# Performance work log

Measured on AMD Instinct MI355X. Metric: run time of the kernel, lower is better.

## Reference

```python
import jax, jax.numpy as jnp
import numpy as np

N_BLOCKS = 4
IN_C = 1024
N_EMBED = 8192
BATCH = 8192
BETA = 1.0
BN_EPS = 1e-5


def _l2norm(t, axis=-1):
    return t / jnp.clip(jnp.linalg.norm(t, axis=axis, keepdims=True), 1e-12, None)


def _mlp_blocks(x, W, b, g, be):
    # n_blocks x (Linear -> BatchNorm1d (batch stats) -> ReLU)
    for i in range(W.shape[0]):
        h = x @ W[i].T + b[i]
        m = h.mean(axis=0)
        v = h.var(axis=0)  # biased var, as torch BN training
        h = (h - m) / jnp.sqrt(v + BN_EPS) * g[i] + be[i]
        x = jax.nn.relu(h)
    return x


def _vq_layer(x, W1, b1, W2, b2):
    return jnp.tanh(x @ W1.T + b1) @ W2.T + b2


def setup_inputs() -> dict:
    key = jax.random.key(0)
    ks = jax.random.split(key, 16)
    w = lambda k, shape: 0.01 * jax.random.normal(k, shape, dtype=jnp.float32)
    d = {
        "x": jax.random.normal(ks[0], (BATCH, IN_C), dtype=jnp.float32),
        "enc_W": w(ks[1], (N_BLOCKS, IN_C, IN_C)),
        "enc_b": jnp.zeros((N_BLOCKS, IN_C), jnp.float32),
        "enc_g": jnp.ones((N_BLOCKS, IN_C), jnp.float32),
        "enc_be": jnp.zeros((N_BLOCKS, IN_C), jnp.float32),
        "enc_vW1": w(ks[2], (IN_C, IN_C)),
        "enc_vb1": jnp.zeros((IN_C,), jnp.float32),
        "enc_vW2": w(ks[3], (IN_C, IN_C)),
        "enc_vb2": jnp.zeros((IN_C,), jnp.float32),
        "dec_W": w(ks[4], (N_BLOCKS, IN_C, IN_C)),
        "dec_b": jnp.zeros((N_BLOCKS, IN_C), jnp.float32),
        "dec_g": jnp.ones((N_BLOCKS, IN_C), jnp.float32),
        "dec_be": jnp.zeros((N_BLOCKS, IN_C), jnp.float32),
        "dec_vW1": w(ks[5], (IN_C, IN_C)),
        "dec_vb1": jnp.zeros((IN_C,), jnp.float32),
        "dec_vW2": w(ks[6], (IN_C, IN_C)),
        "dec_vb2": jnp.zeros((IN_C,), jnp.float32),
        "codebook": _l2norm(jax.random.normal(ks[7], (N_EMBED, IN_C), dtype=jnp.float32)),
    }
    return d


def reference(x, enc_W, enc_b, enc_g, enc_be, enc_vW1, enc_vb1, enc_vW2, enc_vb2,
              dec_W, dec_b, dec_g, dec_be, dec_vW1, dec_vb1, dec_vW2, dec_vb2, codebook):
    # ---- encoder ----
    h = _mlp_blocks(x, enc_W, enc_b, enc_g, enc_be)
    z = _vq_layer(h, enc_vW1, enc_vb1, enc_vW2, enc_vb2)  # [B, D]

    # ---- NormEMA vector quantizer (eval math) ----
    z = _l2norm(z)
    e = _l2norm(codebook)  # [K, D]
    # d(i,k) = |z_i|^2 + |e_k|^2 - 2 z_i . e_k
    d = (jnp.sum(z * z, axis=1, keepdims=True)
         + jnp.sum(e * e, axis=1)[None, :]
         - 2.0 * z @ e.T)  # [B, K]
    idx = jnp.argmin(d, axis=1)
    z_q = e[idx]  # [B, D]
    emb_loss = BETA * jnp.mean((jax.lax.stop_gradient(z_q) - z) ** 2)
    z_q = z + jax.lax.stop_gradient(z_q - z)  # straight-through

    # ---- decoder ----
    h = _mlp_blocks(z_q, dec_W, dec_b, dec_g, dec_be)
    xrec = _vq_layer(h, dec_vW1, dec_vb1, dec_vW2, dec_vb2)
    return xrec, emb_loss
```

## Files before the change

### kernel.cpp

```cpp
#include <hip/hip_runtime.h>

typedef unsigned int u32;
typedef unsigned short u16;
typedef unsigned long long u64;

typedef __attribute__((ext_vector_type(8))) short short8;
typedef __attribute__((ext_vector_type(4))) float f32x4;
typedef __attribute__((ext_vector_type(8))) unsigned short u16x8;
typedef __attribute__((ext_vector_type(4))) unsigned short u16x4;

#define C_DIM 1024
#define B_ROWS 8192
#define N_EMB 8192
#define BN_EPS_C 1e-5f
#define KK 1024

__device__ __forceinline__ u16 f2bf_rne(float x) {
  u32 b = __float_as_uint(x);
  u32 r = b + 0x7fffu + ((b >> 16) & 1u);
  return (u16)(r >> 16);
}
__device__ __forceinline__ float bf2f(u16 h) {
  return __uint_as_float(((u32)h) << 16);
}

__device__ __forceinline__ void gl2lds(const u16* g, u16* l) {
  __builtin_amdgcn_global_load_lds(
      (const __attribute__((address_space(1))) void*)g,
      (__attribute__((address_space(3))) void*)l, 16, 0, 0);
}

__device__ __forceinline__ float block_reduce_sum_256(float v) {
#pragma unroll
  for (int off = 32; off > 0; off >>= 1) v += __shfl_xor(v, off, 64);
  __shared__ float sh[4];
  __syncthreads();
  const int lane = threadIdx.x & 63, w = threadIdx.x >> 6;
  if (lane == 0) sh[w] = v;
  __syncthreads();
  return (sh[0] + sh[1]) + (sh[2] + sh[3]);
}

__device__ __forceinline__ u64 shfl_xor_u64(u64 v, int m) {
  int lo = __shfl_xor((int)(u32)v, m, 64);
  int hi = __shfl_xor((int)(u32)(v >> 32), m, 64);
  return ((u64)(u32)hi << 32) | (u32)lo;
}

__global__ __launch_bounds__(256) void cvt4(
    const float* __restrict__ s0, u16* __restrict__ h0, u16* __restrict__ l0,
    int nb0, const float* __restrict__ s1, u16* __restrict__ h1,
    u16* __restrict__ l1, int nb1, const float* __restrict__ s2,
    u16* __restrict__ h2, u16* __restrict__ l2, int nb2,
    const float* __restrict__ s3, u16* __restrict__ h3, u16* __restrict__ l3) {
  int b = blockIdx.x;
  const float* s;
  u16 *h, *l;
  if (b < nb0) {
    s = s0; h = h0; l = l0;
  } else if (b < nb0 + nb1) {
    b -= nb0; s = s1; h = h1; l = l1;
  } else if (b < nb0 + nb1 + nb2) {
    b -= nb0 + nb1; s = s2; h = h2; l = l2;
  } else {
    b -= nb0 + nb1 + nb2; s = s3; h = h3; l = l3;
  }
  const int i = b * 256 + threadIdx.x;
  const float4 v = ((const float4*)s)[i];
  u16x4 hh, ll;
  hh.x = f2bf_rne(v.x); ll.x = f2bf_rne(v.x - bf2f(hh.x));
  hh.y = f2bf_rne(v.y); ll.y = f2bf_rne(v.y - bf2f(hh.y));
  hh.z = f2bf_rne(v.z); ll.z = f2bf_rne(v.z - bf2f(hh.z));
  hh.w = f2bf_rne(v.w); ll.w = f2bf_rne(v.w - bf2f(hh.w));
  ((u16x4*)h)[i] = hh;
  ((u16x4*)l)[i] = ll;
}

template <int WF32>
__global__ __launch_bounds__(256) void l2norm_ext(const float* __restrict__ in,
                                                  float* __restrict__ outF,
                                                  u16* __restrict__ outH,
                                                  u16* __restrict__ outL,
                                                  float* __restrict__ ssq,
                                                  u64* __restrict__ binit) {
  const int row = blockIdx.x;
  const float4 v = ((const float4*)(in + (size_t)row * C_DIM))[threadIdx.x];
  float ss = v.x * v.x + v.y * v.y + v.z * v.z + v.w * v.w;
  ss = block_reduce_sum_256(ss);
  float nrm = sqrtf(ss);
  nrm = fmaxf(nrm, 1e-12f);
  float4 o;
  o.x = v.x / nrm; o.y = v.y / nrm; o.z = v.z / nrm; o.w = v.w / nrm;
  if (WF32) ((float4*)(outF + (size_t)row * C_DIM))[threadIdx.x] = o;
  u16x4 h, l;
  h.x = f2bf_rne(o.x); l.x = f2bf_rne(o.x - bf2f(h.x));
  h.y = f2bf_rne(o.y); l.y = f2bf_rne(o.y - bf2f(h.y));
  h.z = f2bf_rne(o.z); l.z = f2bf_rne(o.z - bf2f(h.z));
  h.w = f2bf_rne(o.w); l.w = f2bf_rne(o.w - bf2f(h.w));
  ((u16x4*)(outH + (size_t)row * C_DIM))[threadIdx.x] = h;
  ((u16x4*)(outL + (size_t)row * C_DIM))[threadIdx.x] = l;
  float s2 = o.x * o.x + o.y * o.y + o.z * o.z + o.w * o.w;
  s2 = block_reduce_sum_256(s2);
  if (threadIdx.x == 0) {
    ssq[row] = s2;
    if (binit) binit[row] = ~0ull;
  }
}

template <int MODE, int TERMS, int CS, int TB>
__global__ __launch_bounds__(256, (TB ? 4 : 2)) void gemm_bf3(
    const u16* __restrict__ Ahg, const u16* __restrict__ Alg,
    const u16* __restrict__ Bhg, const u16* __restrict__ Blg,
    const float* __restrict__ bias, float* __restrict__ outF,
    u16* __restrict__ outH, u16* __restrict__ outL, float* __restrict__ cs1,
    float* __restrict__ cs2, const float* __restrict__ zz,
    u64* __restrict__ best, int N) {
  __shared__ __align__(16) u16 lds[16384];
  __shared__ float csum[CS ? 4 * 64 * 2 : 1];
  const int tid = threadIdx.x;
  const int lane = tid & 63, w = tid >> 6;
  const int wr = w >> 1, wc = w & 1;
  const int m0 = blockIdx.y * 128, n0 = blockIdx.x * 128;

  const int r0l = w * 32 + (lane >> 2);
  const int r1l = r0l + 16;
  const int c0 = (((lane & 3) ^ ((r0l >> 1) & 3)) << 3);
  const int c1 = (((lane & 3) ^ ((r1l >> 1) & 3)) << 3);
  const u16* pAh0 = Ahg + (size_t)(m0 + r0l) * KK + c0;
  const u16* pAh1 = Ahg + (size_t)(m0 + r1l) * KK + c1;
  const u16* pAl0 = Alg + (size_t)(m0 + r0l) * KK + c0;
  const u16* pAl1 = Alg + (size_t)(m0 + r1l) * KK + c1;
  const u16* pBh0 = Bhg + (size_t)(n0 + r0l) * KK + c0;
  const u16* pBh1 = Bhg + (size_t)(n0 + r1l) * KK + c1;
  const u16* pBl0 = Blg + (size_t)(n0 + r0l) * KK + c0;
  const u16* pBl1 = Blg + (size_t)(n0 + r1l) * KK + c1;
  u16* const db = lds + w * 1024;

  int oa[4], ob[4];
  const int q = lane >> 4;
#pragma unroll
  for (int t = 0; t < 4; ++t) {
    const int ra = wr * 64 + t * 16 + (lane & 15);
    oa[t] = ra * 32 + ((q ^ ((ra >> 1) & 3)) << 3);
    const int rb = wc * 64 + t * 16 + (lane & 15);
    ob[t] = rb * 32 + ((q ^ ((rb >> 1) & 3)) << 3);
  }

  f32x4 acc[4][4];
#pragma unroll
  for (int i = 0; i < 4; ++i)
#pragma unroll
    for (int j = 0; j < 4; ++j) acc[i][j] = (f32x4){0.f, 0.f, 0.f, 0.f};

  for (int k0 = 0; k0 < KK; k0 += 32) {
    __syncthreads();
    gl2lds(pAh0 + k0, db);
    gl2lds(pAh1 + k0, db + 512);
    gl2lds(pAl0 + k0, db + 4096);
    gl2lds(pAl1 + k0, db + 4608);
    gl2lds(pBh0 + k0, db + 8192);
    gl2lds(pBh1 + k0, db + 8704);
    gl2lds(pBl0 + k0, db + 12288);
    gl2lds(pBl1 + k0, db + 12800);
    asm volatile("s_waitcnt vmcnt(0)" ::: "memory");
    __syncthreads();

    if (TB) {
      short8 fa[4], fb[4], fx[4];
#pragma unroll
      for (int t = 0; t < 4; ++t) {
        fa[t] = *(const short8*)(lds + oa[t]);
        fb[t] = *(const short8*)(lds + 8192 + ob[t]);
      }
#pragma unroll
      for (int i = 0; i < 4; ++i)
#pragma unroll
        for (int j = 0; j < 4; ++j)
          acc[i][j] = __builtin_amdgcn_mfma_f32_16x16x32_bf16(
              fa[i], fb[j], acc[i][j], 0, 0, 0);
#pragma unroll
      for (int t = 0; t < 4; ++t)
        fx[t] = *(const short8*)(lds + 12288 + ob[t]);
#pragma unroll
      for (int i = 0; i < 4; ++i)
#pragma unroll
        for (int j = 0; j < 4; ++j)
          acc[i][j] = __builtin_amdgcn_mfma_f32_16x16x32_bf16(
              fa[i], fx[j], acc[i][j], 0, 0, 0);
#pragma unroll
      for (int t = 0; t < 4; ++t)
        fa[t] = *(const short8*)(lds + 4096 + oa[t]);
#pragma unroll
      for (int i = 0; i < 4; ++i)
#pragma unroll
        for (int j = 0; j < 4; ++j)
          acc[i][j] = __builtin_amdgcn_mfma_f32_16x16x32_bf16(
              fa[i], fb[j], acc[i][j], 0, 0, 0);
      if (TERMS == 4) {
#pragma unroll
        for (int i = 0; i < 4; ++i)
#pragma unroll
          for (int j = 0; j < 4; ++j)
            acc[i][j] = __builtin_amdgcn_mfma_f32_16x16x32_bf16(
                fa[i], fx[j], acc[i][j], 0, 0, 0);
      }
    } else {
      short8 ah[4], al[4], bh[4], bl[4];
#pragma unroll
      for (int t = 0; t < 4; ++t) {
        ah[t] = *(const short8*)(lds + oa[t]);
        al[t] = *(const short8*)(lds + 4096 + oa[t]);
        bh[t] = *(const short8*)(lds + 8192 + ob[t]);
        bl[t] = *(const short8*)(lds + 12288 + ob[t]);
      }
#pragma unroll
      for (int i = 0; i < 4; ++i)
#pragma unroll
        for (int j = 0; j < 4; ++j) {
          acc[i][j] = __builtin_amdgcn_mfma_f32_16x16x32_bf16(
              ah[i], bh[j], acc[i][j], 0, 0, 0);
          acc[i][j] = __builtin_amdgcn_mfma_f32_16x16x32_bf16(
              ah[i], bl[j], acc[i][j], 0, 0, 0);
          acc[i][j] = __builtin_amdgcn_mfma_f32_16x16x32_bf16(
              al[i], bh[j], acc[i][j], 0, 0, 0);
          if (TERMS == 4)
            acc[i][j] = __builtin_amdgcn_mfma_f32_16x16x32_bf16(
                al[i], bl[j], acc[i][j], 0, 0, 0);
        }
    }
  }

  const int rbase = m0 + wr * 64 + (lane >> 4) * 4;
  const int cbase = n0 + wc * 64 + (lane & 15);

  if (MODE == 2) {
    float sev[4];
#pragma unroll
    for (int j = 0; j < 4; ++j) sev[j] = bias[cbase + j * 16];
#pragma unroll
    for (int i = 0; i < 4; ++i)
#pragma unroll
      for (int v = 0; v < 4; ++v) {
        const int row = rbase + i * 16 + v;
        const float zr = zz[row];
        u64 bkey = ~0ull;
#pragma unroll
        for (int j = 0; j < 4; ++j) {
          const float d = (zr + sev[j]) - 2.0f * acc[i][j][v];
          const u32 fb2 = __float_as_uint(d);
          const u32 k32 = (fb2 & 0x80000000u) ? ~fb2 : (fb2 | 0x80000000u);
          const u64 key = ((u64)k32 << 32) | (u32)(cbase + j * 16);
          bkey = (key < bkey) ? key : bkey;
        }
#pragma unroll
        for (int mm = 1; mm < 16; mm <<= 1) {
          const u64 o = shfl_xor_u64(bkey, mm);
          bkey = (o < bkey) ? o : bkey;
        }
        if ((lane & 15) == 0) atomicMin(best + row, bkey);
      }
  } else {
    float bb[4];
#pragma unroll
    for (int j = 0; j < 4; ++j) bb[j] = bias[cbase + j * 16];
    float s[4] = {0.f, 0.f, 0.f, 0.f}, ss[4] = {0.f, 0.f, 0.f, 0.f};
#pragma unroll
    for (int i = 0; i < 4; ++i)
#pragma unroll
      for (int j = 0; j < 4; ++j)
#pragma unroll
        for (int v = 0; v < 4; ++v) {
          const int row = rbase + i * 16 + v;
          const int col = cbase + j * 16;
          float val = acc[i][j][v] + bb[j];
          if (MODE == 1) {
            val = tanhf(val);
            const u16 h = f2bf_rne(val);
            outH[(size_t)row * N + col] = h;
            outL[(size_t)row * N + col] = f2bf_rne(val - bf2f(h));
          } else {
            outF[(size_t)row * N + col] = val;
            if (CS) {
              s[j] += val;
              ss[j] += val * val;
            }
          }
        }
    if (CS) {
#pragma unroll
      for (int j = 0; j < 4; ++j) {
        s[j] += __shfl_xor(s[j], 16, 64);
        s[j] += __shfl_xor(s[j], 32, 64);
        ss[j] += __shfl_xor(ss[j], 16, 64);
        ss[j] += __shfl_xor(ss[j], 32, 64);
      }
      if (lane < 16) {
#pragma unroll
        for (int j = 0; j < 4; ++j) {
          csum[(w * 64 + j * 16 + lane) * 2 + 0] = s[j];
          csum[(w * 64 + j * 16 + lane) * 2 + 1] = ss[j];
        }
      }
      __syncthreads();
      if (tid < 128) {
        const int col = tid;
        const int wcc = col >> 6, idx = col & 63;
        const float S = csum[(wcc * 64 + idx) * 2 + 0] +
                        csum[((2 + wcc) * 64 + idx) * 2 + 0];
        const float SS = csum[(wcc * 64 + idx) * 2 + 1] +
                         csum[((2 + wcc) * 64 + idx) * 2 + 1];
        cs1[(size_t)blockIdx.y * C_DIM + n0 + col] = S;
        cs2[(size_t)blockIdx.y * C_DIM + n0 + col] = SS;
      }
    }
  }
}

__global__ __launch_bounds__(256) void bn_stats2(const float* __restrict__ cs1,
                                                 const float* __restrict__ cs2,
                                                 const float* __restrict__ g,
                                                 float* __restrict__ mean,
                                                 float* __restrict__ scale) {
  const int c = blockIdx.x * 256 + threadIdx.x;
  float s = 0.f, ss = 0.f;
  for (int i = 0; i < 64; ++i) {
    s += cs1[i * C_DIM + c];
    ss += cs2[i * C_DIM + c];
  }
  const float m = s * (1.0f / 8192.0f);
  const float v = ss * (1.0f / 8192.0f) - m * m;
  mean[c] = m;
  scale[c] = g[c] / sqrtf(v + BN_EPS_C);
}

__global__ __launch_bounds__(256) void bn_relu_cvt(
    const float* __restrict__ t, const float* __restrict__ mean,
    const float* __restrict__ scale, const float* __restrict__ be,
    u16* __restrict__ outH, u16* __restrict__ outL) {
  const int i = blockIdx.x * 256 + threadIdx.x;
  const int c4 = i & 255;
  const float4 v = ((const float4*)t)[i];
  const float4 m = ((const float4*)mean)[c4];
  const float4 sc = ((const float4*)scale)[c4];
  const float4 b = ((const float4*)be)[c4];
  float4 r;
  r.x = fmaxf((v.x - m.x) * sc.x + b.x, 0.f);
  r.y = fmaxf((v.y - m.y) * sc.y + b.y, 0.f);
  r.z = fmaxf((v.z - m.z) * sc.z + b.z, 0.f);
  r.w = fmaxf((v.w - m.w) * sc.w + b.w, 0.f);
  u16x4 h, l;
  h.x = f2bf_rne(r.x); l.x = f2bf_rne(r.x - bf2f(h.x));
  h.y = f2bf_rne(r.y); l.y = f2bf_rne(r.y - bf2f(h.y));
  h.z = f2bf_rne(r.z); l.z = f2bf_rne(r.z - bf2f(h.z));
  h.w = f2bf_rne(r.w); l.w = f2bf_rne(r.w - bf2f(h.w));
  ((u16x4*)outH)[i] = h;
  ((u16x4*)outL)[i] = l;
}

__global__ __launch_bounds__(256) void gather_zq_cvt(
    const float* __restrict__ z, const u16* __restrict__ eh,
    const u16* __restrict__ el, const u64* __restrict__ best,
    u16* __restrict__ zqh, u16* __restrict__ zql, float* __restrict__ rowp) {
  const int row = blockIdx.x;
  const u32 idx = (u32)(best[row] & 0xffffffffu);
  const float4 zv = ((const float4*)(z + (size_t)row * C_DIM))[threadIdx.x];
  const u16x4 evh = ((const u16x4*)(eh + (size_t)idx * C_DIM))[threadIdx.x];
  const u16x4 evl = ((const u16x4*)(el + (size_t)idx * C_DIM))[threadIdx.x];
  float4 ev;
  ev.x = bf2f(evh.x) + bf2f(evl.x);
  ev.y = bf2f(evh.y) + bf2f(evl.y);
  ev.z = bf2f(evh.z) + bf2f(evl.z);
  ev.w = bf2f(evh.w) + bf2f(evl.w);
  float4 d, o;
  d.x = ev.x - zv.x; d.y = ev.y - zv.y; d.z = ev.z - zv.z; d.w = ev.w - zv.w;
  o.x = zv.x + d.x; o.y = zv.y + d.y; o.z = zv.z + d.z; o.w = zv.w + d.w;
  u16x4 h, l;
  h.x = f2bf_rne(o.x); l.x = f2bf_rne(o.x - bf2f(h.x));
  h.y = f2bf_rne(o.y); l.y = f2bf_rne(o.y - bf2f(h.y));
  h.z = f2bf_rne(o.z); l.z = f2bf_rne(o.z - bf2f(h.z));
  h.w = f2bf_rne(o.w); l.w = f2bf_rne(o.w - bf2f(h.w));
  ((u16x4*)(zqh + (size_t)row * C_DIM))[threadIdx.x] = h;
  ((u16x4*)(zql + (size_t)row * C_DIM))[threadIdx.x] = l;
  float ss = d.x * d.x + d.y * d.y + d.z * d.z + d.w * d.w;
  ss = block_reduce_sum_256(ss);
  if (threadIdx.x == 0) rowp[row] = ss;
}

__global__ __launch_bounds__(256) void embloss_fin(const float* __restrict__ rowp,
                                                   float* __restrict__ out) {
  float s = 0.f;
  for (int i = threadIdx.x; i < B_ROWS; i += 256) s += rowp[i];
  s = block_reduce_sum_256(s);
  if (threadIdx.x == 0) out[0] = s * (1.0f / (8192.0f * 1024.0f));
}

extern "C" void kernel_launch(void* const* d_in, const int* in_sizes, int n_in,
                              void* d_out, int out_size, void* d_ws,
                              size_t ws_size, hipStream_t stream) {
  const float* x = (const float*)d_in[0];
  const float* enc_W = (const float*)d_in[1];
  const float* enc_b = (const float*)d_in[2];
  const float* enc_g = (const float*)d_in[3];
  const float* enc_be = (const float*)d_in[4];
  const float* enc_vW1 = (const float*)d_in[5];
  const float* enc_vb1 = (const float*)d_in[6];
  const float* enc_vW2 = (const float*)d_in[7];
  const float* enc_vb2 = (const float*)d_in[8];
  const float* dec_W = (const float*)d_in[9];
  const float* dec_b = (const float*)d_in[10];
  const float* dec_g = (const float*)d_in[11];
  const float* dec_be = (const float*)d_in[12];
  const float* dec_vW1 = (const float*)d_in[13];
  const float* dec_vb1 = (const float*)d_in[14];
  const float* dec_vW2 = (const float*)d_in[15];
  const float* dec_vb2 = (const float*)d_in[16];
  const float* cb = (const float*)d_in[17];

  const size_t NE = (size_t)B_ROWS * C_DIM;
  const size_t WN = (size_t)C_DIM * C_DIM;
  float* ws = (float*)d_ws;
  float* R1 = ws;
  float* R2 = R1 + NE;
  float* R3 = R2 + NE;
  float* R4 = R3 + NE;
  float* se = R4 + NE;
  float* zz = se + N_EMB;
  u64* best = (u64*)(zz + B_ROWS);
  float* cs1 = (float*)(best + B_ROWS);
  float* cs2 = cs1 + 64 * C_DIM;
  float* mean = cs2 + 64 * C_DIM;
  float* scal = mean + C_DIM;
  float* rowp = scal + C_DIM;

  u16* wa = (u16*)R4;
  u16* ehi = (u16*)R4;
  u16* elo = ehi + NE;
  u16* xh = (u16*)R2;
  u16* xl = xh + NE;
  u16* aH = (u16*)R2;
  u16* aL = aH + NE;
  u16* bH = (u16*)R3;
  u16* bL = bH + NE;
  u16* zhi = (u16*)R2;
  u16* zlo = zhi + NE;
  float* zf = R1;

  float* xrec = (float*)d_out;
  float* loss = xrec + NE;

  const dim3 blk(256);
  const dim3 gemmGrid(C_DIM / 128, B_ROWS / 128);
  const dim3 distGrid(N_EMB / 128, B_ROWS / 128);
  const dim3 s2Grid(C_DIM / 256);
  const dim3 brGrid(B_ROWS * C_DIM / 1024);

  cvt4<<<dim3(4096 + 1024 + 1024 + 8192), blk, 0, stream>>>(
      enc_W, wa, wa + 4 * WN, 4096, enc_vW1, wa + 8 * WN, wa + 9 * WN, 1024,
      enc_vW2, wa + 10 * WN, wa + 11 * WN, 1024, x, xh, xl);

  gemm_bf3<0, 4, 1, 0><<<gemmGrid, blk, 0, stream>>>(
      xh, xl, wa, wa + 4 * WN, enc_b, R1, nullptr, nullptr, cs1, cs2, nullptr,
      nullptr, C_DIM);
  bn_stats2<<<s2Grid, blk, 0, stream>>>(cs1, cs2, enc_g, mean, scal);
  bn_relu_cvt<<<brGrid, blk, 0, stream>>>(R1, mean, scal, enc_be, bH, bL);

  gemm_bf3<0, 4, 1, 0><<<gemmGrid, blk, 0, stream>>>(
      bH, bL, wa + WN, wa + 5 * WN, enc_b + C_DIM, R1, nullptr, nullptr, cs1,
      cs2, nullptr, nullptr, C_DIM);
  bn_stats2<<<s2Grid, blk, 0, stream>>>(cs1, cs2, enc_g + C_DIM, mean, scal);
  bn_relu_cvt<<<brGrid, blk, 0, stream>>>(R1, mean, scal, enc_be + C_DIM, aH,
                                          aL);

  gemm_bf3<0, 4, 1, 0><<<gemmGrid, blk, 0, stream>>>(
      aH, aL, wa + 2 * WN, wa + 6 * WN, enc_b + 2 * C_DIM, R1, nullptr,
      nullptr, cs1, cs2, nullptr, nullptr, C_DIM);
  bn_stats2<<<s2Grid, blk, 0, stream>>>(cs1, cs2, enc_g + 2 * C_DIM, mean,
                                        scal);
  bn_relu_cvt<<<brGrid, blk, 0, stream>>>(R1, mean, scal, enc_be + 2 * C_DIM,
                                          bH, bL);

  gemm_bf3<0, 4, 1, 0><<<gemmGrid, blk, 0, stream>>>(
      bH, bL, wa + 3 * WN, wa + 7 * WN, enc_b + 3 * C_DIM, R1, nullptr,
      nullptr, cs1, cs2, nullptr, nullptr, C_DIM);
  bn_stats2<<<s2Grid, blk, 0, stream>>>(cs1, cs2, enc_g + 3 * C_DIM, mean,
                                        scal);
  bn_relu_cvt<<<brGrid, blk, 0, stream>>>(R1, mean, scal, enc_be + 3 * C_DIM,
                                          aH, aL);

  gemm_bf3<1, 4, 0, 0><<<gemmGrid, blk, 0, stream>>>(
      aH, aL, wa + 8 * WN, wa + 9 * WN, enc_vb1, nullptr, bH, bL, nullptr,
      nullptr, nullptr, nullptr, C_DIM);
  gemm_bf3<0, 4, 0, 0><<<gemmGrid, blk, 0, stream>>>(
      bH, bL, wa + 10 * WN, wa + 11 * WN, enc_vb2, zf, nullptr, nullptr,
      nullptr, nullptr, nullptr, nullptr, C_DIM);

  l2norm_ext<0><<<N_EMB, blk, 0, stream>>>(cb, nullptr, ehi, elo, se, nullptr);
  l2norm_ext<1><<<B_ROWS, blk, 0, stream>>>(zf, zf, zhi, zlo, zz, best);
  gemm_bf3<2, 3, 0, 1><<<distGrid, blk, 0, stream>>>(
      zhi, zlo, ehi, elo, se, nullptr, nullptr, nullptr, nullptr, nullptr, zz,
      best, N_EMB);
  gather_zq_cvt<<<B_ROWS, blk, 0, stream>>>(zf, ehi, elo, best, bH, bL, rowp);
  embloss_fin<<<1, blk, 0, stream>>>(rowp, loss);

  cvt4<<<dim3(4096 + 1024 + 1024), blk, 0, stream>>>(
      dec_W, wa, wa + 4 * WN, 4096, dec_vW1, wa + 8 * WN, wa + 9 * WN, 1024,
      dec_vW2, wa + 10 * WN, wa + 11 * WN, 1024, nullptr, nullptr, nullptr);

  gemm_bf3<0, 3, 1, 0><<<gemmGrid, blk, 0, stream>>>(
      bH, bL, wa, wa + 4 * WN, dec_b, R1, nullptr, nullptr, cs1, cs2, nullptr,
      nullptr, C_DIM);
  bn_stats2<<<s2Grid, blk, 0, stream>>>(cs1, cs2, dec_g, mean, scal);
  bn_relu_cvt<<<brGrid, blk, 0, stream>>>(R1, mean, scal, dec_be, aH, aL);

  gemm_bf3<0, 3, 1, 0><<<gemmGrid, blk, 0, stream>>>(
      aH, aL, wa + WN, wa + 5 * WN, dec_b + C_DIM, R1, nullptr, nullptr, cs1,
      cs2, nullptr, nullptr, C_DIM);
  bn_stats2<<<s2Grid, blk, 0, stream>>>(cs1, cs2, dec_g + C_DIM, mean, scal);
  bn_relu_cvt<<<brGrid, blk, 0, stream>>>(R1, mean, scal, dec_be + C_DIM, bH,
                                          bL);

  gemm_bf3<0, 3, 1, 0><<<gemmGrid, blk, 0, stream>>>(
      bH, bL, wa + 2 * WN, wa + 6 * WN, dec_b + 2 * C_DIM, R1, nullptr,
      nullptr, cs1, cs2, nullptr, nullptr, C_DIM);
  bn_stats2<<<s2Grid, blk, 0, stream>>>(cs1, cs2, dec_g + 2 * C_DIM, mean,
                                        scal);
  bn_relu_cvt<<<brGrid, blk, 0, stream>>>(R1, mean, scal, dec_be + 2 * C_DIM,
                                          aH, aL);

  gemm_bf3<0, 3, 1, 0><<<gemmGrid, blk, 0, stream>>>(
      aH, aL, wa + 3 * WN, wa + 7 * WN, dec_b + 3 * C_DIM, R1, nullptr,
      nullptr, cs1, cs2, nullptr, nullptr, C_DIM);
  bn_stats2<<<s2Grid, blk, 0, stream>>>(cs1, cs2, dec_g + 3 * C_DIM, mean,
                                        scal);
  bn_relu_cvt<<<brGrid, blk, 0, stream>>>(R1, mean, scal, dec_be + 3 * C_DIM,
                                          bH, bL);

  gemm_bf3<1, 3, 0, 0><<<gemmGrid, blk, 0, stream>>>(
      bH, bL, wa + 8 * WN, wa + 9 * WN, dec_vb1, nullptr, aH, aL, nullptr,
      nullptr, nullptr, nullptr, C_DIM);
  gemm_bf3<0, 3, 0, 0><<<gemmGrid, blk, 0, stream>>>(
      aH, aL, wa + 10 * WN, wa + 11 * WN, dec_vb2, xrec, nullptr, nullptr,
      nullptr, nullptr, nullptr, nullptr, C_DIM);
}
```

Before: 1.278 ms.

## Overlap next K-tile global-to-LDS loads with MFMA compute in split-bf16 GEMM

Restructures the GEMM main loop so that, once all LDS fragments for the current K-tile are in registers, a barrier is taken and the next tile's global_load_lds is issued before the MFMA chain runs. The wait on vmcnt moves to the end of the iteration, so memory latency can hide behind the matrix math instead of stalling before each tile. It still uses a single LDS buffer, relying on register-held fragments to free the buffer early. This costs extra barriers and keeps more fragments live in registers.

```diff
diff --git a/kernel.cpp b/kernel.cpp
--- a/kernel.cpp
+++ b/kernel.cpp
@@ -14,6 +14,7 @@
 #define N_EMB 8192
 #define BN_EPS_C 1e-5f
 #define KK 1024
+#define NKT 32
 
 __device__ __forceinline__ u16 f2bf_rne(float x) {
   u32 b = __float_as_uint(x);
@@ -136,6 +137,17 @@
   const u16* pBl1 = Blg + (size_t)(n0 + r1l) * KK + c1;
   u16* const db = lds + w * 1024;
 
+  auto STAGE = [&](int ko) {
+    gl2lds(pAh0 + ko, db);
+    gl2lds(pAh1 + ko, db + 512);
+    gl2lds(pAl0 + ko, db + 4096);
+    gl2lds(pAl1 + ko, db + 4608);
+    gl2lds(pBh0 + ko, db + 8192);
+    gl2lds(pBh1 + ko, db + 8704);
+    gl2lds(pBl0 + ko, db + 12288);
+    gl2lds(pBl1 + ko, db + 12800);
+  };
+
   int oa[4], ob[4];
   const int q = lane >> 4;
 #pragma unroll
@@ -152,19 +164,11 @@
 #pragma unroll
     for (int j = 0; j < 4; ++j) acc[i][j] = (f32x4){0.f, 0.f, 0.f, 0.f};
 
-  for (int k0 = 0; k0 < KK; k0 += 32) {
-    __syncthreads();
-    gl2lds(pAh0 + k0, db);
-    gl2lds(pAh1 + k0, db + 512);
-    gl2lds(pAl0 + k0, db + 4096);
-    gl2lds(pAl1 + k0, db + 4608);
-    gl2lds(pBh0 + k0, db + 8192);
-    gl2lds(pBh1 + k0, db + 8704);
-    gl2lds(pBl0 + k0, db + 12288);
-    gl2lds(pBl1 + k0, db + 12800);
-    asm volatile("s_waitcnt vmcnt(0)" ::: "memory");
-    __syncthreads();
-
+  STAGE(0);
+  asm volatile("s_waitcnt vmcnt(0)" ::: "memory");
+  __syncthreads();
+
+  for (int kt = 0; kt < NKT; ++kt) {
     if (TB) {
       short8 fa[4], fb[4], fx[4];
 #pragma unroll
@@ -190,6 +194,10 @@
 #pragma unroll
       for (int t = 0; t < 4; ++t)
         fa[t] = *(const short8*)(lds + 4096 + oa[t]);
+      asm volatile("s_waitcnt lgkmcnt(0)" ::: "memory");
+      __builtin_amdgcn_sched_barrier(0);
+      __builtin_amdgcn_s_barrier();
+      if (kt + 1 < NKT) STAGE((kt + 1) * 32);
 #pragma unroll
       for (int i = 0; i < 4; ++i)
 #pragma unroll
@@ -213,6 +221,10 @@
         bh[t] = *(const short8*)(lds + 8192 + ob[t]);
         bl[t] = *(const short8*)(lds + 12288 + ob[t]);
       }
+      asm volatile("s_waitcnt lgkmcnt(0)" ::: "memory");
+      __builtin_amdgcn_sched_barrier(0);
+      __builtin_amdgcn_s_barrier();
+      if (kt + 1 < NKT) STAGE((kt + 1) * 32);
 #pragma unroll
       for (int i = 0; i < 4; ++i)
 #pragma unroll
@@ -227,6 +239,11 @@
             acc[i][j] = __builtin_amdgcn_mfma_f32_16x16x32_bf16(
                 al[i], bl[j], acc[i][j], 0, 0, 0);
         }
+    }
+    if (kt + 1 < NKT) {
+      asm volatile("s_waitcnt vmcnt(0)" ::: "memory");
+      __builtin_amdgcn_sched_barrier(0);
+      __builtin_amdgcn_s_barrier();
     }
   }
 
```

Measured after the change: 1.345 ms. 1.05x slower.
